# Optimization experiments

Measured on AMD Instinct MI355X. Metric: run time of the kernel, lower is better.

Reference implementation:

```python
import jax, jax.numpy as jnp
import numpy as np

FEAT = 64      # feature_dim
HEADS = 4      # n_head
LATENT = 256   # latent_dim
G = 128        # num graphs
NPG = 150      # nodes per graph (<=180 for one-hot positions)
N = G * NPG    # 19200 nodes
E = N * 12     # 230400 edges (excl. self loops)
POS = 180      # one-hot position classes
SLOPE = 0.2    # PyG GATConv leaky_relu negative slope


def gat_conv(x, src, dst, W, att_s, att_d, bias):
    """PyG GATConv (concat heads, self loops already appended to src/dst)."""
    n = x.shape[0]
    h = (x @ W).reshape(n, HEADS, FEAT)                 # [N,H,F]
    a_s = jnp.sum(h * att_s, axis=-1)                   # [N,H]
    a_d = jnp.sum(h * att_d, axis=-1)                   # [N,H]
    e = jax.nn.leaky_relu(a_s[src] + a_d[dst], SLOPE)   # [E,H] per-edge logits
    m = jax.ops.segment_max(e, dst, num_segments=n)     # segment softmax over dst
    ex = jnp.exp(e - m[dst])
    s = jax.ops.segment_sum(ex, dst, num_segments=n)
    alpha = ex / (s[dst] + 1e-16)
    out = jax.ops.segment_sum(h[src] * alpha[:, :, None], dst, num_segments=n)
    return out.reshape(n, HEADS * FEAT) + bias


def setup_inputs() -> dict:
    key = jax.random.key(0)
    ks = jax.random.split(key, 20)

    def p(k, shape, fan_in):
        return jax.random.normal(k, shape, jnp.float32) / np.sqrt(fan_in).astype(np.float32)

    z = jax.random.normal(ks[0], (G, LATENT), jnp.float32)
    src = jax.random.randint(ks[1], (E,), 0, N, jnp.int32)
    dst = (src + jax.random.randint(ks[2], (E,), 1, N, jnp.int32)) % N  # no self loops
    edge_index = jnp.stack([src, dst])
    batch = jnp.repeat(jnp.arange(G, dtype=jnp.int32), NPG)

    in1 = FEAT + POS
    in2 = FEAT * HEADS
    inp = dict(z=z, edge_index=edge_index, batch=batch, num_graphs=G)
    inp.update(
        W0=p(ks[3], (LATENT, FEAT), LATENT), b0=jnp.zeros(FEAT, jnp.float32),
        W1=p(ks[4], (in1, HEADS * FEAT), in1),
        as1=p(ks[5], (HEADS, FEAT), FEAT), ad1=p(ks[6], (HEADS, FEAT), FEAT),
        bb1=jnp.zeros(HEADS * FEAT, jnp.float32),
        W2=p(ks[7], (in2, HEADS * FEAT), in2),
        as2=p(ks[8], (HEADS, FEAT), FEAT), ad2=p(ks[9], (HEADS, FEAT), FEAT),
        bb2=jnp.zeros(HEADS * FEAT, jnp.float32),
        W3=p(ks[10], (in2, HEADS * FEAT), in2),
        as3=p(ks[11], (HEADS, FEAT), FEAT), ad3=p(ks[12], (HEADS, FEAT), FEAT),
        bb3=jnp.zeros(HEADS * FEAT, jnp.float32),
        Wg=p(ks[13], (in2, FEAT), in2), bg=jnp.zeros(FEAT, jnp.float32),
        Wf=p(ks[14], (FEAT, 5), FEAT), bf=jnp.zeros(5, jnp.float32),
    )
    return inp


def reference(z, edge_index, batch, num_graphs,
              W0, b0, W1, as1, ad1, bb1, W2, as2, ad2, bb2,
              W3, as3, ad3, bb3, Wg, bg, Wf, bf):
    n = batch.shape[0]
    x = z @ W0 + b0                                    # dec_feature_init
    x = x[batch]                                       # broadcast graph latent to nodes
    # node_order_within_batch (batch is sorted)
    counts = jax.ops.segment_sum(jnp.ones_like(batch), batch, num_segments=num_graphs)
    starts = jnp.cumsum(counts) - counts
    order = jnp.arange(n, dtype=batch.dtype) - starts[batch]
    pos = jax.nn.one_hot(order, POS, dtype=x.dtype)
    x = jax.nn.relu(jnp.concatenate([x, pos], axis=1))
    # GATConv adds self loops by default
    loops = jnp.arange(n, dtype=edge_index.dtype)
    src = jnp.concatenate([edge_index[0], loops])
    dst = jnp.concatenate([edge_index[1], loops])
    x = jax.nn.relu(gat_conv(x, src, dst, W1, as1, ad1, bb1))
    x = jax.nn.relu(gat_conv(x, src, dst, W2, as2, ad2, bb2))
    x = jax.nn.relu(gat_conv(x, src, dst, W3, as3, ad3, bb3))
    x = jax.nn.relu(x @ Wg + bg)                       # dec_geo
    return x @ Wf + bf                                 # fc_geo -> [N,5]
```

## Files before the change

### kernel.cpp

```cpp
#include <hip/hip_runtime.h>
#include <hip/hip_fp16.h>

#define GNUM 128
#define HEADS 4
#define FEAT 64
#define CH 256
#define LAT 256
#define SLOPE 0.2f
#define CAP 64

typedef _Float16 h16;
typedef __attribute__((ext_vector_type(4))) _Float16 half4;
typedef __attribute__((ext_vector_type(8))) _Float16 half8;
typedef __attribute__((ext_vector_type(4))) float floatx4;

__device__ __forceinline__ float lrelu(float x) { return fmaxf(x, SLOPE * x); }

__global__ __launch_bounds__(256) void k_setup(const int* __restrict__ batch, int* __restrict__ cnt,
                                               int* __restrict__ starts, int n,
                                               const float* __restrict__ W2, const float* __restrict__ W3,
                                               const float* __restrict__ Wg, h16* __restrict__ W2T,
                                               h16* __restrict__ W3T, h16* __restrict__ WgT,
                                               const float* __restrict__ z, const float* __restrict__ W0,
                                               const float* __restrict__ b0, const float* __restrict__ W1,
                                               float* __restrict__ A) {
  __shared__ float red[4][FEAT];
  __shared__ float xzs[FEAT];
  int bx = blockIdx.x, t = threadIdx.x;
  if (bx < 576) {
    int idx = bx * 256 + t;
    if (idx < n) {
      cnt[idx] = 0;
      int b = batch[idx];
      if (idx == 0 || batch[idx - 1] != b) starts[b] = idx;
    }
    if (idx < 65536) {
      int kb = idx >> 13, rem = idx & 8191, j = rem >> 8, nn = rem & 255;
      W2T[kb * 8192 + nn * 32 + j] = (h16)W2[(kb * 32 + j) * 256 + nn];
    } else if (idx < 131072) {
      int l = idx - 65536;
      int kb = l >> 13, rem = l & 8191, j = rem >> 8, nn = rem & 255;
      W3T[kb * 8192 + nn * 32 + j] = (h16)W3[(kb * 32 + j) * 256 + nn];
    } else {
      int l = idx - 131072;
      int kb = l >> 11, rem = l & 2047, j = rem >> 6, nn = rem & 63;
      WgT[kb * 2048 + nn * 32 + j] = (h16)Wg[(kb * 32 + j) * 64 + nn];
    }
  } else {
    int g = bx - 576;
    int f = t & 63, kq = t >> 6;
    float acc = 0.f;
    for (int k = kq * 64; k < kq * 64 + 64; ++k) acc += z[g * LAT + k] * W0[k * FEAT + f];
    red[kq][f] = acc;
    __syncthreads();
    if (kq == 0)
      xzs[f] = fmaxf(red[0][f] + red[1][f] + red[2][f] + red[3][f] + b0[f], 0.f);
    __syncthreads();
    float a2 = 0.f;
#pragma unroll 16
    for (int k = 0; k < FEAT; ++k) a2 += xzs[k] * W1[k * CH + t];
    A[g * CH + t] = a2;
  }
}

__global__ __launch_bounds__(256) void k_H1(const float* __restrict__ A, const float* __restrict__ W1,
                                            const int* __restrict__ batch, const int* __restrict__ starts,
                                            const float* __restrict__ att_s, const float* __restrict__ att_d,
                                            h16* __restrict__ H16, float* __restrict__ a_s,
                                            float* __restrict__ a_d) {
  int n = blockIdx.x, c = threadIdx.x;
  int g = batch[n];
  int p = n - starts[g];
  float val = A[g * CH + c] + W1[(FEAT + p) * CH + c];
  H16[(size_t)n * CH + c] = (h16)val;
  float ps = val * att_s[c];
  float pd = val * att_d[c];
#pragma unroll
  for (int w = 1; w < 64; w <<= 1) {
    ps += __shfl_xor(ps, w, 64);
    pd += __shfl_xor(pd, w, 64);
  }
  if ((c & 63) == 0) {
    int h = c >> 6;
    a_s[n * 4 + h] = ps;
    a_d[n * 4 + h] = pd;
  }
}

__global__ void k_scatter(const int* __restrict__ src, const int* __restrict__ dst,
                          int* __restrict__ cnt, int* __restrict__ bucket, int e) {
  int i = blockIdx.x * blockDim.x + threadIdx.x;
  if (i < e) {
    int d = dst[i];
    int p = atomicAdd(&cnt[d], 1);
    if (p < CAP) bucket[d * CAP + p] = src[i];
  }
}

__global__ __launch_bounds__(256) void k_galpha(const h16* __restrict__ H16, const float* __restrict__ a_s,
                                                const float* __restrict__ a_d, const float* __restrict__ bias,
                                                const int* __restrict__ cnt, const int* __restrict__ bucket,
                                                h16* __restrict__ X16) {
  __shared__ float wsh[4][CAP][4];
  __shared__ int bsh[4][CAP];
  int wv = threadIdx.x >> 6, lane = threadIdx.x & 63;
  int n = blockIdx.x * 4 + wv;
  int c = min(cnt[n], CAP);
  bool valid = lane < c;
  int sc = valid ? bucket[n * CAP + lane] : n;
  if (valid) bsh[wv][lane] = sc;
  float4 ea4 = *(const float4*)(a_s + (size_t)sc * 4);
  float4 sn4 = *(const float4*)(a_s + (size_t)n * 4);
  float4 dn4 = *(const float4*)(a_d + (size_t)n * 4);
  float ea[4] = {ea4.x, ea4.y, ea4.z, ea4.w};
  float sn[4] = {sn4.x, sn4.y, sn4.z, sn4.w};
  float dn[4] = {dn4.x, dn4.y, dn4.z, dn4.w};
  float asf[4];
#pragma unroll
  for (int h = 0; h < 4; ++h) {
    float e = valid ? lrelu(ea[h] + dn[h]) : -1e30f;
    float es = lrelu(sn[h] + dn[h]);
    float m = e;
#pragma unroll
    for (int sh = 1; sh < 64; sh <<= 1) m = fmaxf(m, __shfl_xor(m, sh, 64));
    m = fmaxf(m, es);
    float wgt = valid ? __expf(e - m) : 0.f;
    float ws = __expf(es - m);
    float s = wgt;
#pragma unroll
    for (int sh = 1; sh < 64; sh <<= 1) s += __shfl_xor(s, sh, 64);
    s += ws;
    float inv = 1.f / (s + 1e-16f);
    if (valid) wsh[wv][lane][h] = wgt * inv;
    asf[h] = ws * inv;
  }
  __syncthreads();
  int hh = lane >> 4;
  int fo = lane * 4;
  half4 hv = *(const half4*)(H16 + (size_t)n * CH + fo);
  float a_self = asf[hh];
  float acc0 = a_self * (float)hv[0];
  float acc1 = a_self * (float)hv[1];
  float acc2 = a_self * (float)hv[2];
  float acc3 = a_self * (float)hv[3];
  for (int j = 0; j < c; ++j) {
    int s2 = bsh[wv][j];
    half4 hs = *(const half4*)(H16 + (size_t)s2 * CH + fo);
    float wj = wsh[wv][j][hh];
    acc0 += wj * (float)hs[0];
    acc1 += wj * (float)hs[1];
    acc2 += wj * (float)hs[2];
    acc3 += wj * (float)hs[3];
  }
  float4 b4 = *(const float4*)(bias + fo);
  half4 o;
  o[0] = (h16)fmaxf(acc0 + b4.x, 0.f);
  o[1] = (h16)fmaxf(acc1 + b4.y, 0.f);
  o[2] = (h16)fmaxf(acc2 + b4.z, 0.f);
  o[3] = (h16)fmaxf(acc3 + b4.w, 0.f);
  *(half4*)(X16 + (size_t)n * CH + fo) = o;
}

__global__ __launch_bounds__(256) void k_gemm(const h16* __restrict__ X16, const h16* __restrict__ WT,
                                              const float* __restrict__ att_s, const float* __restrict__ att_d,
                                              h16* __restrict__ H16, float* __restrict__ a_s,
                                              float* __restrict__ a_d) {
  __shared__ __align__(16) char smem[64 * 264 * 2];
  h16* As = (h16*)smem;
  h16* Bs = (h16*)(smem + 64 * 40 * 2);
  h16* Ht = (h16*)smem;
  int t = threadIdx.x;
  int w = t >> 6, lane = t & 63;
  int quad = lane >> 4, l15 = lane & 15;
  int row0 = blockIdx.x * 64;
  floatx4 acc[4][4];
#pragma unroll
  for (int i = 0; i < 4; ++i)
#pragma unroll
    for (int j = 0; j < 4; ++j) acc[i][j] = (floatx4){0.f, 0.f, 0.f, 0.f};
  int srow = t >> 2, sseg = t & 3;
  for (int kb = 0; kb < 8; ++kb) {
    __syncthreads();
    *(half8*)&As[srow * 40 + sseg * 8] =
        *(const half8*)(X16 + (size_t)(row0 + srow) * CH + kb * 32 + sseg * 8);
    {
      const h16* src = WT + kb * 8192 + t * 32;
      h16* dst = &Bs[t * 40];
      *(half8*)(dst + 0)  = *(const half8*)(src + 0);
      *(half8*)(dst + 8)  = *(const half8*)(src + 8);
      *(half8*)(dst + 16) = *(const half8*)(src + 16);
      *(half8*)(dst + 24) = *(const half8*)(src + 24);
    }
    __syncthreads();
    half8 af[4], bf[4];
#pragma unroll
    for (int mt = 0; mt < 4; ++mt) af[mt] = *(const half8*)&As[(mt * 16 + l15) * 40 + quad * 8];
#pragma unroll
    for (int nt = 0; nt < 4; ++nt)
      bf[nt] = *(const half8*)&Bs[(w * 64 + nt * 16 + l15) * 40 + quad * 8];
#pragma unroll
    for (int mt = 0; mt < 4; ++mt)
#pragma unroll
      for (int nt = 0; nt < 4; ++nt)
        acc[mt][nt] = __builtin_amdgcn_mfma_f32_16x16x32_f16(af[mt], bf[nt], acc[mt][nt], 0, 0, 0);
  }
  __syncthreads();
#pragma unroll
  for (int mt = 0; mt < 4; ++mt)
#pragma unroll
    for (int nt = 0; nt < 4; ++nt)
#pragma unroll
      for (int r = 0; r < 4; ++r)
        Ht[(mt * 16 + quad * 4 + r) * 264 + w * 64 + nt * 16 + l15] = (h16)acc[mt][nt][r];
  float asv[4], adv[4];
#pragma unroll
  for (int nt = 0; nt < 4; ++nt) {
    asv[nt] = att_s[w * FEAT + nt * 16 + l15];
    adv[nt] = att_d[w * FEAT + nt * 16 + l15];
  }
#pragma unroll
  for (int mt = 0; mt < 4; ++mt)
#pragma unroll
    for (int r = 0; r < 4; ++r) {
      float ps = acc[mt][0][r] * asv[0] + acc[mt][1][r] * asv[1] +
                 acc[mt][2][r] * asv[2] + acc[mt][3][r] * asv[3];
      float pd = acc[mt][0][r] * adv[0] + acc[mt][1][r] * adv[1] +
                 acc[mt][2][r] * adv[2] + acc[mt][3][r] * adv[3];
#pragma unroll
      for (int sh = 1; sh < 16; sh <<= 1) {
        ps += __shfl_xor(ps, sh, 16);
        pd += __shfl_xor(pd, sh, 16);
      }
      if (l15 == 0) {
        int row = row0 + mt * 16 + quad * 4 + r;
        a_s[row * 4 + w] = ps;
        a_d[row * 4 + w] = pd;
      }
    }
  __syncthreads();
  {
    const h16* srcr = &Ht[srow * 264 + sseg * 64];
    h16* dstr = H16 + (size_t)(row0 + srow) * CH + sseg * 64;
#pragma unroll
    for (int i = 0; i < 8; ++i) *(half8*)(dstr + i * 8) = *(const half8*)(srcr + i * 8);
  }
}

__global__ __launch_bounds__(256) void k_head(const h16* __restrict__ X16, const h16* __restrict__ WgT,
                                              const float* __restrict__ bg, const float* __restrict__ Wf,
                                              const float* __restrict__ bfv, float* __restrict__ out) {
  __shared__ __align__(16) char smem[64 * 68 * 4];
  h16* As = (h16*)smem;
  h16* Bs = (h16*)(smem + 64 * 40 * 2);
  float* ytile = (float*)smem;
  __shared__ float WfS[FEAT * 5];
  int t = threadIdx.x;
  int w = t >> 6, lane = t & 63;
  int quad = lane >> 4, l15 = lane & 15;
  int row0 = blockIdx.x * 64;
  for (int i = t; i < FEAT * 5; i += 256) WfS[i] = Wf[i];
  floatx4 acc[4];
#pragma unroll
  for (int mt = 0; mt < 4; ++mt) acc[mt] = (floatx4){0.f, 0.f, 0.f, 0.f};
  int srow = t >> 2, sseg = t & 3;
  for (int kb = 0; kb < 8; ++kb) {
    __syncthreads();
    *(half8*)&As[srow * 40 + sseg * 8] =
        *(const half8*)(X16 + (size_t)(row0 + srow) * CH + kb * 32 + sseg * 8);
    *(half8*)&Bs[srow * 40 + sseg * 8] =
        *(const half8*)(WgT + kb * 2048 + srow * 32 + sseg * 8);
    __syncthreads();
    half8 af[4], bf;
#pragma unroll
    for (int mt = 0; mt < 4; ++mt) af[mt] = *(const half8*)&As[(mt * 16 + l15) * 40 + quad * 8];
    bf = *(const half8*)&Bs[(w * 16 + l15) * 40 + quad * 8];
#pragma unroll
    for (int mt = 0; mt < 4; ++mt)
      acc[mt] = __builtin_amdgcn_mfma_f32_16x16x32_f16(af[mt], bf, acc[mt], 0, 0, 0);
  }
  __syncthreads();
  int col = w * 16 + l15;
  float bgv = bg[col];
#pragma unroll
  for (int mt = 0; mt < 4; ++mt)
#pragma unroll
    for (int r = 0; r < 4; ++r)
      ytile[(mt * 16 + quad * 4 + r) * 68 + col] = fmaxf(acc[mt][r] + bgv, 0.f);
  __syncthreads();
  for (int i = t; i < 64 * 5; i += 256) {
    int row = i / 5, o = i % 5;
    float s = bfv[o];
#pragma unroll
    for (int k = 0; k < FEAT; ++k) s += ytile[row * 68 + k] * WfS[k * 5 + o];
    out[(size_t)(row0 + row) * 5 + o] = s;
  }
}

static inline size_t alignup(size_t x) { return (x + 255) & ~(size_t)255; }

extern "C" void kernel_launch(void* const* d_in, const int* in_sizes, int n_in,
                              void* d_out, int out_size, void* d_ws, size_t ws_size,
                              hipStream_t stream) {
  (void)n_in; (void)out_size; (void)ws_size;
  const float* z   = (const float*)d_in[0];
  const int* edge  = (const int*)d_in[1];
  const int* batch = (const int*)d_in[2];
  const float* W0  = (const float*)d_in[4];
  const float* b0  = (const float*)d_in[5];
  const float* W1  = (const float*)d_in[6];
  const float* as1 = (const float*)d_in[7];
  const float* ad1 = (const float*)d_in[8];
  const float* bb1 = (const float*)d_in[9];
  const float* W2  = (const float*)d_in[10];
  const float* as2 = (const float*)d_in[11];
  const float* ad2 = (const float*)d_in[12];
  const float* bb2 = (const float*)d_in[13];
  const float* W3  = (const float*)d_in[14];
  const float* as3 = (const float*)d_in[15];
  const float* ad3 = (const float*)d_in[16];
  const float* bb3 = (const float*)d_in[17];
  const float* Wg  = (const float*)d_in[18];
  const float* bg  = (const float*)d_in[19];
  const float* Wf  = (const float*)d_in[20];
  const float* bfv = (const float*)d_in[21];
  float* out = (float*)d_out;

  const int E = in_sizes[1] / 2;
  const int N = in_sizes[2];
  const int* srcI = edge;
  const int* dstI = edge + E;

  char* w = (char*)d_ws;
  auto carve = [&](size_t bytes) { void* p = (void*)w; w += alignup(bytes); return p; };
  int* starts  = (int*)carve((size_t)GNUM * 4);
  int* cnt     = (int*)carve((size_t)N * 4);
  int* bucket  = (int*)carve((size_t)N * CAP * 4);
  float* A     = (float*)carve((size_t)GNUM * CH * 4);
  float* a_s   = (float*)carve((size_t)N * 4 * 4);
  float* a_d   = (float*)carve((size_t)N * 4 * 4);
  h16* W2T     = (h16*)carve((size_t)CH * CH * 2);
  h16* W3T     = (h16*)carve((size_t)CH * CH * 2);
  h16* WgT     = (h16*)carve((size_t)CH * FEAT * 2);
  h16* H16     = (h16*)carve((size_t)N * CH * 2);
  h16* X16     = (h16*)carve((size_t)N * CH * 2);

  int eb256 = (E + 255) / 256;

  hipLaunchKernelGGL(k_setup, dim3(576 + GNUM), dim3(256), 0, stream,
                     batch, cnt, starts, N, W2, W3, Wg, W2T, W3T, WgT, z, W0, b0, W1, A);
  hipLaunchKernelGGL(k_H1, dim3(N), dim3(256), 0, stream, A, W1, batch, starts, as1, ad1, H16, a_s, a_d);
  hipLaunchKernelGGL(k_scatter, dim3(eb256), dim3(256), 0, stream, srcI, dstI, cnt, bucket, E);

  hipLaunchKernelGGL(k_galpha, dim3(N / 4), dim3(256), 0, stream, H16, a_s, a_d, bb1, cnt, bucket, X16);
  hipLaunchKernelGGL(k_gemm, dim3(N / 64), dim3(256), 0, stream, X16, W2T, as2, ad2, H16, a_s, a_d);
  hipLaunchKernelGGL(k_galpha, dim3(N / 4), dim3(256), 0, stream, H16, a_s, a_d, bb2, cnt, bucket, X16);
  hipLaunchKernelGGL(k_gemm, dim3(N / 64), dim3(256), 0, stream, X16, W3T, as3, ad3, H16, a_s, a_d);
  hipLaunchKernelGGL(k_galpha, dim3(N / 4), dim3(256), 0, stream, H16, a_s, a_d, bb3, cnt, bucket, X16);
  hipLaunchKernelGGL(k_head, dim3(N / 64), dim3(256), 0, stream, X16, WgT, bg, Wf, bfv, out);
}
```

Before: 275.5 us.

## Precompute layer-1 attention terms, register-prefetch GEMM tiles, widen row tiles to 80

```diff
diff --git a/kernel.cpp b/kernel.cpp
--- a/kernel.cpp
+++ b/kernel.cpp
@@ -8,6 +8,7 @@
 #define LAT 256
 #define SLOPE 0.2f
 #define CAP 64
+#define POSMAX 180
 
 typedef _Float16 h16;
 typedef __attribute__((ext_vector_type(4))) _Float16 half4;
@@ -23,7 +24,10 @@
                                                h16* __restrict__ W3T, h16* __restrict__ WgT,
                                                const float* __restrict__ z, const float* __restrict__ W0,
                                                const float* __restrict__ b0, const float* __restrict__ W1,
-                                               float* __restrict__ A) {
+                                               const float* __restrict__ as1, const float* __restrict__ ad1,
+                                               float* __restrict__ A, float* __restrict__ asg,
+                                               float* __restrict__ adg, float* __restrict__ asp,
+                                               float* __restrict__ adp) {
   __shared__ float red[4][FEAT];
   __shared__ float xzs[FEAT];
   int bx = blockIdx.x, t = threadIdx.x;
@@ -46,7 +50,7 @@
       int kb = l >> 11, rem = l & 2047, j = rem >> 6, nn = rem & 63;
       WgT[kb * 2048 + nn * 32 + j] = (h16)Wg[(kb * 32 + j) * 64 + nn];
     }
-  } else {
+  } else if (bx < 576 + GNUM) {
     int g = bx - 576;
     int f = t & 63, kq = t >> 6;
     float acc = 0.f;
@@ -60,30 +64,63 @@
 #pragma unroll 16
     for (int k = 0; k < FEAT; ++k) a2 += xzs[k] * W1[k * CH + t];
     A[g * CH + t] = a2;
+    float ps = a2 * as1[t], pd = a2 * ad1[t];
+#pragma unroll
+    for (int sh = 1; sh < 64; sh <<= 1) {
+      ps += __shfl_xor(ps, sh, 64);
+      pd += __shfl_xor(pd, sh, 64);
+    }
+    if ((t & 63) == 0) {
+      asg[g * 4 + (t >> 6)] = ps;
+      adg[g * 4 + (t >> 6)] = pd;
+    }
+  } else {
+    int p = bx - (576 + GNUM);
+    float wv = W1[(size_t)(FEAT + p) * CH + t];
+    float ps = wv * as1[t], pd = wv * ad1[t];
+#pragma unroll
+    for (int sh = 1; sh < 64; sh <<= 1) {
+      ps += __shfl_xor(ps, sh, 64);
+      pd += __shfl_xor(pd, sh, 64);
+    }
+    if ((t & 63) == 0) {
+      asp[p * 4 + (t >> 6)] = ps;
+      adp[p * 4 + (t >> 6)] = pd;
+    }
   }
 }
 
 __global__ __launch_bounds__(256) void k_H1(const float* __restrict__ A, const float* __restrict__ W1,
                                             const int* __restrict__ batch, const int* __restrict__ starts,
-                                            const float* __restrict__ att_s, const float* __restrict__ att_d,
+                                            const float* __restrict__ asg, const float* __restrict__ adg,
+                                            const float* __restrict__ asp, const float* __restrict__ adp,
                                             h16* __restrict__ H16, float* __restrict__ a_s,
-                                            float* __restrict__ a_d) {
-  int n = blockIdx.x, c = threadIdx.x;
-  int g = batch[n];
-  int p = n - starts[g];
-  float val = A[g * CH + c] + W1[(FEAT + p) * CH + c];
-  H16[(size_t)n * CH + c] = (h16)val;
-  float ps = val * att_s[c];
-  float pd = val * att_d[c];
-#pragma unroll
-  for (int w = 1; w < 64; w <<= 1) {
-    ps += __shfl_xor(ps, w, 64);
-    pd += __shfl_xor(pd, w, 64);
-  }
-  if ((c & 63) == 0) {
-    int h = c >> 6;
-    a_s[n * 4 + h] = ps;
-    a_d[n * 4 + h] = pd;
+                                            float* __restrict__ a_d, int n) {
+  int t = threadIdx.x;
+  int row = blockIdx.x * 8 + (t >> 5);
+  if (row < n) {
+    int g = batch[row];
+    int p = row - starts[g];
+    int c0 = (t & 31) * 8;
+    const float* ap = A + g * CH + c0;
+    const float* wp = W1 + (size_t)(FEAT + p) * CH + c0;
+    float4 a0 = *(const float4*)ap;
+    float4 a1 = *(const float4*)(ap + 4);
+    float4 w0v = *(const float4*)wp;
+    float4 w1v = *(const float4*)(wp + 4);
+    half8 o;
+    o[0] = (h16)(a0.x + w0v.x); o[1] = (h16)(a0.y + w0v.y);
+    o[2] = (h16)(a0.z + w0v.z); o[3] = (h16)(a0.w + w0v.w);
+    o[4] = (h16)(a1.x + w1v.x); o[5] = (h16)(a1.y + w1v.y);
+    o[6] = (h16)(a1.z + w1v.z); o[7] = (h16)(a1.w + w1v.w);
+    *(half8*)(H16 + (size_t)row * CH + c0) = o;
+  }
+  int idx = blockIdx.x * 256 + t;
+  if (idx < n * 4) {
+    int nn = idx >> 2, h = idx & 3;
+    int g2 = batch[nn], p2 = nn - starts[g2];
+    a_s[idx] = asg[g2 * 4 + h] + asp[p2 * 4 + h];
+    a_d[idx] = adg[g2 * 4 + h] + adp[p2 * 4 + h];
   }
 }
 
@@ -143,14 +180,21 @@
   float acc1 = a_self * (float)hv[1];
   float acc2 = a_self * (float)hv[2];
   float acc3 = a_self * (float)hv[3];
-  for (int j = 0; j < c; ++j) {
-    int s2 = bsh[wv][j];
+  if (c > 0) {
+    int s2 = bsh[wv][0];
     half4 hs = *(const half4*)(H16 + (size_t)s2 * CH + fo);
-    float wj = wsh[wv][j][hh];
-    acc0 += wj * (float)hs[0];
-    acc1 += wj * (float)hs[1];
-    acc2 += wj * (float)hs[2];
-    acc3 += wj * (float)hs[3];
+    for (int j = 0; j < c; ++j) {
+      float wj = wsh[wv][j][hh];
+      half4 hc = hs;
+      if (j + 1 < c) {
+        int s3 = bsh[wv][j + 1];
+        hs = *(const half4*)(H16 + (size_t)s3 * CH + fo);
+      }
+      acc0 += wj * (float)hc[0];
+      acc1 += wj * (float)hc[1];
+      acc2 += wj * (float)hc[2];
+      acc3 += wj * (float)hc[3];
+    }
   }
   float4 b4 = *(const float4*)(bias + fo);
   half4 o;
@@ -165,48 +209,61 @@
                                               const float* __restrict__ att_s, const float* __restrict__ att_d,
                                               h16* __restrict__ H16, float* __restrict__ a_s,
                                               float* __restrict__ a_d) {
-  __shared__ __align__(16) char smem[64 * 264 * 2];
+  __shared__ __align__(16) char smem[80 * 264 * 2];
   h16* As = (h16*)smem;
-  h16* Bs = (h16*)(smem + 64 * 40 * 2);
+  h16* Bs = (h16*)(smem + 6400);
   h16* Ht = (h16*)smem;
   int t = threadIdx.x;
   int w = t >> 6, lane = t & 63;
   int quad = lane >> 4, l15 = lane & 15;
-  int row0 = blockIdx.x * 64;
-  floatx4 acc[4][4];
-#pragma unroll
-  for (int i = 0; i < 4; ++i)
+  int row0 = blockIdx.x * 80;
+  int arow = t >> 2, aseg = t & 3;
+  floatx4 acc[5][4];
+#pragma unroll
+  for (int i = 0; i < 5; ++i)
 #pragma unroll
     for (int j = 0; j < 4; ++j) acc[i][j] = (floatx4){0.f, 0.f, 0.f, 0.f};
-  int srow = t >> 2, sseg = t & 3;
+  half8 ra0, ra1, rb0, rb1, rb2, rb3;
+  ra0 = *(const half8*)(X16 + (size_t)(row0 + arow) * CH + aseg * 8);
+  if (t < 64) ra1 = *(const half8*)(X16 + (size_t)(row0 + arow + 64) * CH + aseg * 8);
+  {
+    const h16* s = WT + t * 32;
+    rb0 = *(const half8*)(s + 0);  rb1 = *(const half8*)(s + 8);
+    rb2 = *(const half8*)(s + 16); rb3 = *(const half8*)(s + 24);
+  }
   for (int kb = 0; kb < 8; ++kb) {
     __syncthreads();
-    *(half8*)&As[srow * 40 + sseg * 8] =
-        *(const half8*)(X16 + (size_t)(row0 + srow) * CH + kb * 32 + sseg * 8);
+    *(half8*)&As[arow * 40 + aseg * 8] = ra0;
+    if (t < 64) *(half8*)&As[(arow + 64) * 40 + aseg * 8] = ra1;
     {
-      const h16* src = WT + kb * 8192 + t * 32;
-      h16* dst = &Bs[t * 40];
-      *(half8*)(dst + 0)  = *(const half8*)(src + 0);
-      *(half8*)(dst + 8)  = *(const half8*)(src + 8);
-      *(half8*)(dst + 16) = *(const half8*)(src + 16);
-      *(half8*)(dst + 24) = *(const half8*)(src + 24);
-    }
-    __syncthreads();
-    half8 af[4], bf[4];
-#pragma unroll
-    for (int mt = 0; mt < 4; ++mt) af[mt] = *(const half8*)&As[(mt * 16 + l15) * 40 + quad * 8];
+      h16* bd = &Bs[t * 40];
+      *(half8*)(bd + 0) = rb0;  *(half8*)(bd + 8) = rb1;
+      *(half8*)(bd + 16) = rb2; *(half8*)(bd + 24) = rb3;
+    }
+    __syncthreads();
+    if (kb < 7) {
+      ra0 = *(const half8*)(X16 + (size_t)(row0 + arow) * CH + (kb + 1) * 32 + aseg * 8);
+      if (t < 64)
+        ra1 = *(const half8*)(X16 + (size_t)(row0 + arow + 64) * CH + (kb + 1) * 32 + aseg * 8);
+      const h16* s = WT + (kb + 1) * 8192 + t * 32;
+      rb0 = *(const half8*)(s + 0);  rb1 = *(const half8*)(s + 8);
+      rb2 = *(const half8*)(s + 16); rb3 = *(const half8*)(s + 24);
+    }
+    half8 af[5], bf[4];
+#pragma unroll
+    for (int mt = 0; mt < 5; ++mt) af[mt] = *(const half8*)&As[(mt * 16 + l15) * 40 + quad * 8];
 #pragma unroll
     for (int nt = 0; nt < 4; ++nt)
       bf[nt] = *(const half8*)&Bs[(w * 64 + nt * 16 + l15) * 40 + quad * 8];
 #pragma unroll
-    for (int mt = 0; mt < 4; ++mt)
+    for (int mt = 0; mt < 5; ++mt)
 #pragma unroll
       for (int nt = 0; nt < 4; ++nt)
         acc[mt][nt] = __builtin_amdgcn_mfma_f32_16x16x32_f16(af[mt], bf[nt], acc[mt][nt], 0, 0, 0);
   }
   __syncthreads();
 #pragma unroll
-  for (int mt = 0; mt < 4; ++mt)
+  for (int mt = 0; mt < 5; ++mt)
 #pragma unroll
     for (int nt = 0; nt < 4; ++nt)
 #pragma unroll
@@ -219,7 +276,7 @@
     adv[nt] = att_d[w * FEAT + nt * 16 + l15];
   }
 #pragma unroll
-  for (int mt = 0; mt < 4; ++mt)
+  for (int mt = 0; mt < 5; ++mt)
 #pragma unroll
     for (int r = 0; r < 4; ++r) {
       float ps = acc[mt][0][r] * asv[0] + acc[mt][1][r] * asv[1] +
@@ -238,9 +295,9 @@
       }
     }
   __syncthreads();
-  {
-    const h16* srcr = &Ht[srow * 264 + sseg * 64];
-    h16* dstr = H16 + (size_t)(row0 + srow) * CH + sseg * 64;
+  for (int rr = t >> 2; rr < 80; rr += 64) {
+    const h16* srcr = &Ht[rr * 264 + aseg * 64];
+    h16* dstr = H16 + (size_t)(row0 + rr) * CH + aseg * 64;
 #pragma unroll
     for (int i = 0; i < 8; ++i) *(half8*)(dstr + i * 8) = *(const half8*)(srcr + i * 8);
   }
@@ -249,45 +306,54 @@
 __global__ __launch_bounds__(256) void k_head(const h16* __restrict__ X16, const h16* __restrict__ WgT,
                                               const float* __restrict__ bg, const float* __restrict__ Wf,
                                               const float* __restrict__ bfv, float* __restrict__ out) {
-  __shared__ __align__(16) char smem[64 * 68 * 4];
+  __shared__ __align__(16) char smem[80 * 68 * 4];
   h16* As = (h16*)smem;
-  h16* Bs = (h16*)(smem + 64 * 40 * 2);
+  h16* Bs = (h16*)(smem + 6400);
   float* ytile = (float*)smem;
   __shared__ float WfS[FEAT * 5];
   int t = threadIdx.x;
   int w = t >> 6, lane = t & 63;
   int quad = lane >> 4, l15 = lane & 15;
-  int row0 = blockIdx.x * 64;
+  int row0 = blockIdx.x * 80;
+  int arow = t >> 2, aseg = t & 3;
   for (int i = t; i < FEAT * 5; i += 256) WfS[i] = Wf[i];
-  floatx4 acc[4];
-#pragma unroll
-  for (int mt = 0; mt < 4; ++mt) acc[mt] = (floatx4){0.f, 0.f, 0.f, 0.f};
-  int srow = t >> 2, sseg = t & 3;
+  floatx4 acc[5];
+#pragma unroll
+  for (int mt = 0; mt < 5; ++mt) acc[mt] = (floatx4){0.f, 0.f, 0.f, 0.f};
+  half8 ra0, ra1, rb;
+  ra0 = *(const half8*)(X16 + (size_t)(row0 + arow) * CH + aseg * 8);
+  if (t < 64) ra1 = *(const half8*)(X16 + (size_t)(row0 + arow + 64) * CH + aseg * 8);
+  rb = *(const half8*)(WgT + arow * 32 + aseg * 8);
   for (int kb = 0; kb < 8; ++kb) {
     __syncthreads();
-    *(half8*)&As[srow * 40 + sseg * 8] =
-        *(const half8*)(X16 + (size_t)(row0 + srow) * CH + kb * 32 + sseg * 8);
-    *(half8*)&Bs[srow * 40 + sseg * 8] =
-        *(const half8*)(WgT + kb * 2048 + srow * 32 + sseg * 8);
-    __syncthreads();
-    half8 af[4], bf;
-#pragma unroll
-    for (int mt = 0; mt < 4; ++mt) af[mt] = *(const half8*)&As[(mt * 16 + l15) * 40 + quad * 8];
-    bf = *(const half8*)&Bs[(w * 16 + l15) * 40 + quad * 8];
-#pragma unroll
-    for (int mt = 0; mt < 4; ++mt)
-      acc[mt] = __builtin_amdgcn_mfma_f32_16x16x32_f16(af[mt], bf, acc[mt], 0, 0, 0);
+    *(half8*)&As[arow * 40 + aseg * 8] = ra0;
+    if (t < 64) *(half8*)&As[(arow + 64) * 40 + aseg * 8] = ra1;
+    *(half8*)&Bs[arow * 40 + aseg * 8] = rb;
+    __syncthreads();
+    if (kb < 7) {
+      ra0 = *(const half8*)(X16 + (size_t)(row0 + arow) * CH + (kb + 1) * 32 + aseg * 8);
+      if (t < 64)
+        ra1 = *(const half8*)(X16 + (size_t)(row0 + arow + 64) * CH + (kb + 1) * 32 + aseg * 8);
+      rb = *(const half8*)(WgT + (kb + 1) * 2048 + arow * 32 + aseg * 8);
+    }
+    half8 af[5], bfr;
+#pragma unroll
+    for (int mt = 0; mt < 5; ++mt) af[mt] = *(const half8*)&As[(mt * 16 + l15) * 40 + quad * 8];
+    bfr = *(const half8*)&Bs[(w * 16 + l15) * 40 + quad * 8];
+#pragma unroll
+    for (int mt = 0; mt < 5; ++mt)
+      acc[mt] = __builtin_amdgcn_mfma_f32_16x16x32_f16(af[mt], bfr, acc[mt], 0, 0, 0);
   }
   __syncthreads();
   int col = w * 16 + l15;
   float bgv = bg[col];
 #pragma unroll
-  for (int mt = 0; mt < 4; ++mt)
+  for (int mt = 0; mt < 5; ++mt)
 #pragma unroll
     for (int r = 0; r < 4; ++r)
       ytile[(mt * 16 + quad * 4 + r) * 68 + col] = fmaxf(acc[mt][r] + bgv, 0.f);
   __syncthreads();
-  for (int i = t; i < 64 * 5; i += 256) {
+  for (int i = t; i < 80 * 5; i += 256) {
     int row = i / 5, o = i % 5;
     float s = bfv[o];
 #pragma unroll
@@ -338,6 +404,10 @@
   float* A     = (float*)carve((size_t)GNUM * CH * 4);
   float* a_s   = (float*)carve((size_t)N * 4 * 4);
   float* a_d   = (float*)carve((size_t)N * 4 * 4);
+  float* asg   = (float*)carve((size_t)GNUM * 4 * 4);
+  float* adg   = (float*)carve((size_t)GNUM * 4 * 4);
+  float* asp   = (float*)carve((size_t)POSMAX * 4 * 4);
+  float* adp   = (float*)carve((size_t)POSMAX * 4 * 4);
   h16* W2T     = (h16*)carve((size_t)CH * CH * 2);
   h16* W3T     = (h16*)carve((size_t)CH * CH * 2);
   h16* WgT     = (h16*)carve((size_t)CH * FEAT * 2);
@@ -346,15 +416,17 @@
 
   int eb256 = (E + 255) / 256;
 
-  hipLaunchKernelGGL(k_setup, dim3(576 + GNUM), dim3(256), 0, stream,
-                     batch, cnt, starts, N, W2, W3, Wg, W2T, W3T, WgT, z, W0, b0, W1, A);
-  hipLaunchKernelGGL(k_H1, dim3(N), dim3(256), 0, stream, A, W1, batch, starts, as1, ad1, H16, a_s, a_d);
+  hipLaunchKernelGGL(k_setup, dim3(576 + GNUM + POSMAX), dim3(256), 0, stream,
+                     batch, cnt, starts, N, W2, W3, Wg, W2T, W3T, WgT, z, W0, b0, W1,
+                     as1, ad1, A, asg, adg, asp, adp);
+  hipLaunchKernelGGL(k_H1, dim3(N / 8), dim3(256), 0, stream,
+                     A, W1, batch, starts, asg, adg, asp, adp, H16, a_s, a_d, N);
   hipLaunchKernelGGL(k_scatter, dim3(eb256), dim3(256), 0, stream, srcI, dstI, cnt, bucket, E);
 
   hipLaunchKernelGGL(k_galpha, dim3(N / 4), dim3(256), 0, stream, H16, a_s, a_d, bb1, cnt, bucket, X16);
-  hipLaunchKernelGGL(k_gemm, dim3(N / 64), dim3(256), 0, stream, X16, W2T, as2, ad2, H16, a_s, a_d);
+  hipLaunchKernelGGL(k_gemm, dim3(N / 80), dim3(256), 0, stream, X16, W2T, as2, ad2, H16, a_s, a_d);
   hipLaunchKernelGGL(k_galpha, dim3(N / 4), dim3(256), 0, stream, H16, a_s, a_d, bb2, cnt, bucket, X16);
-  hipLaunchKernelGGL(k_gemm, dim3(N / 64), dim3(256), 0, stream, X16, W3T, as3, ad3, H16, a_s, a_d);
+  hipLaunchKernelGGL(k_gemm, dim3(N / 80), dim3(256), 0, stream, X16, W3T, as3, ad3, H16, a_s, a_d);
   hipLaunchKernelGGL(k_galpha, dim3(N / 4), dim3(256), 0, stream, H16, a_s, a_d, bb3, cnt, bucket, X16);
-  hipLaunchKernelGGL(k_head, dim3(N / 64), dim3(256), 0, stream, X16, WgT, bg, Wf, bfv, out);
-}
+  hipLaunchKernelGGL(k_head, dim3(N / 80), dim3(256), 0, stream, X16, WgT, bg, Wf, bfv, out);
+}
```

Result: no change. 280.7 us (+1.9%).
